# Kernel optimization log

Hardware: AMD Instinct MI355X
Metric: run time of the kernel (lower is better)

## Reference

```python
import jax, jax.numpy as jnp
import numpy as np

# Module config (matches init_kwargs)
SHAPE = (96, 128, 128)   # (D, H, W)
NUM_LAYERS = 2
K, S, P, DIL = 3, 2, 1, 1  # kernel, stride, padding, dilation (dilation=1)


def _sparse_maxpool(feat, mask):
    """One SparseMaxPool3d layer on a densified sparse tensor.

    feat: [B, D, H, W, C] float, inactive sites hold dtype-min
    mask: [B, D, H, W, 1] float 0/1 activity mask
    Max is taken only over ACTIVE input sites in each window (spconv semantics);
    an output site is active iff any input in its window is active.
    """
    neg = jnp.finfo(feat.dtype).min
    window = (1, K, K, K, 1)
    strides = (1, S, S, S, 1)
    pad = [(0, 0), (P, P), (P, P), (P, P), (0, 0)]
    masked = jnp.where(mask > 0, feat, neg)
    pooled = jax.lax.reduce_window(masked, neg, jax.lax.max, window, strides, pad)
    mask_out = jax.lax.reduce_window(mask, jnp.array(0, feat.dtype).item() * 0.0,
                                     jax.lax.max, window, strides, pad)
    return pooled, mask_out


def setup_inputs() -> dict:
    key = jax.random.key(0)
    k1, k2, k3, k4, k5 = jax.random.split(key, 5)
    N, C, B = 200000, 32, 2
    D, H, W = SHAPE
    features = jax.random.normal(k1, (N, C), dtype=jnp.float32)
    b = jax.random.randint(k2, (N,), 0, B)
    z = jax.random.randint(k3, (N,), 0, D)
    y = jax.random.randint(k4, (N,), 0, H)
    x = jax.random.randint(k5, (N,), 0, W)
    coors = jnp.stack([b, z, y, x], axis=1).astype(jnp.int32)
    return {"features": features, "coors": coors, "batch_size": B}


def reference(features, coors, batch_size):
    D, H, W = SHAPE
    C = features.shape[1]
    b, z, y, x = coors[:, 0], coors[:, 1], coors[:, 2], coors[:, 3]
    neg = jnp.finfo(features.dtype).min
    # Densify the sparse tensor (duplicate coords resolved by max, inactive = -inf)
    dense = jnp.full((batch_size, D, H, W, C), neg, features.dtype)
    dense = dense.at[b, z, y, x].max(features)
    mask = jnp.zeros((batch_size, D, H, W, 1), features.dtype).at[b, z, y, x].set(1.0)
    for _ in range(NUM_LAYERS):
        dense, mask = _sparse_maxpool(dense, mask)
    # Equivalent of SparseConvTensor.dense(): inactive output sites are 0
    return jnp.where(mask > 0, dense, jnp.zeros((), features.dtype))
```

## Files before the change

kernel.cpp:

```cpp
#include <hip/hip_runtime.h>
#include <cfloat>
#include <cstdint>

#define B_    2
#define OD    24
#define OH    32
#define OW    32
#define NC    32
#define NBINS (B_ * OD * OH * OW)
#define LINE  16
#define CAPR  15
#define OVF_CAP 100000
#define SCAN_T 1024
#define CHUNK  (NBINS / SCAN_T)

#define TZ 4
#define TY 4
#define TX 2
#define TCELLS (TZ*TY*TX)
#define NTZ (OD/TZ)
#define NTY (OH/TY)
#define NTX (OW/TX)
#define NTILES (B_*NTZ*NTY*NTX)
#define NBZ (TZ+1)
#define NBY (TY+1)
#define NBX (TX+1)
#define NB  (NBZ*NBY*NBX)
#define LIST_CAP 1280
#define DUMP (TCELLS*NC)


__global__ void k_zero(int* __restrict__ lines, int* __restrict__ ovf_n) {
    int i = blockIdx.x * blockDim.x + threadIdx.x;
    if (i < NBINS) lines[i * LINE] = 0;
    if (i == 0) *ovf_n = 0;
}

__global__ __launch_bounds__(256) void k_bin(const int* __restrict__ coors,
                                             int* __restrict__ lines,
                                             int* __restrict__ ovf_n,
                                             int2* __restrict__ ovf, int N) {
    int i = blockIdx.x * blockDim.x + threadIdx.x;
    if (i >= N) return;
    int4 cc = reinterpret_cast<const int4*>(coors)[i];
    int bin = (((cc.x * OD + (cc.y >> 2)) * OH + (cc.z >> 2)) * OW + (cc.w >> 2));
    int mask = 0xFF;
    if (!(cc.y & 3)) mask &= 0x55;
    if (!(cc.z & 3)) mask &= 0x33;
    if (!(cc.w & 3)) mask &= 0x0F;
    int rec = (i << 8) | mask;
    int pos = atomicAdd(&lines[bin * LINE], 1);
    if (pos < CAPR) {
        lines[bin * LINE + 1 + pos] = rec;
    } else {
        int o = atomicAdd(ovf_n, 1);
        if (o < OVF_CAP) ovf[o] = make_int2(bin, rec);
    }
}

__device__ __forceinline__ unsigned xform(float f) {
    unsigned u = __float_as_uint(f);
    return u ^ ((unsigned)((int)u >> 31) | 0x80000000u);
}
__device__ __forceinline__ float unxform(unsigned t) {
    return (t == 0u) ? 0.0f
           : __uint_as_float((t >> 31) ? (t ^ 0x80000000u) : ~t);
}

__global__ __launch_bounds__(512) void k_tile(const float* __restrict__ feat,
                                              const int* __restrict__ lines,
                                              const int* __restrict__ ovf_n,
                                              const int2* __restrict__ ovf,
                                              float4* __restrict__ out4) {
    __shared__ unsigned sm_out[TCELLS * NC + 32];
    __shared__ int2 list[LIST_CAP];
    __shared__ int sm_cursor;

    const int tid = threadIdx.x;
    int bid = blockIdx.x;
    int b  = (bid >= NTZ * NTY * NTX) ? 1 : 0;
    int r  = bid - b * (NTZ * NTY * NTX);
    int ti = r >> 7;
    int rr = r & 127;
    int tj = rr >> 4;
    int tl = rr & 15;
    const int tz0 = ti * TZ, ty0 = tj * TY, tx0 = tl * TX;

    if (tid == 0) sm_cursor = 0;
    for (int v = tid; v < TCELLS * NC + 32; v += 512) sm_out[v] = 0u;
    __syncthreads();

    if (tid < NB) {
        int rz  = tid / (NBY * NBX);
        int rem = tid - rz * (NBY * NBX);
        int ry  = rem / NBX;
        int rx  = rem - ry * NBX;
        int bz = tz0 - 1 + rz, by = ty0 - 1 + ry, bx = tx0 - 1 + rx;
        if ((bz | by | bx) >= 0) {
            int bin = ((b * OD + bz) * OH + by) * OW + bx;
            const int4* lp = (const int4*)(lines + bin * LINE);
            int4 q0 = lp[0], q1 = lp[1], q2 = lp[2], q3 = lp[3];
            int rbuf[16];
            *(int4*)&rbuf[0]  = q0; *(int4*)&rbuf[4]  = q1;
            *(int4*)&rbuf[8]  = q2; *(int4*)&rbuf[12] = q3;
            int cnt = rbuf[0]; if (cnt > CAPR) cnt = CAPR;
            int bi = rz - 1, bj = ry - 1, bl = rx - 1;
            int vm = 0xFF;
            if (bi < 0) vm &= 0xAA;  if (bi > TZ - 2) vm &= 0x55;
            if (bj < 0) vm &= 0xCC;  if (bj > TY - 2) vm &= 0x33;
            if (bl < 0) vm &= 0xF0;  if (bl > TX - 2) vm &= 0x0F;
            int cb = bi * (TY * TX) + bj * TX + bl;
#pragma unroll
            for (int rs = 0; rs < CAPR; ++rs) {
                if (rs < cnt) {
                    int rec = rbuf[rs + 1];
                    int fm = rec & vm & 0xFF;
                    if (fm) {
                        int pos = atomicAdd(&sm_cursor, 1);
                        if (pos < LIST_CAP)
                            list[pos] = make_int2((rec & ~0xFF) | fm, cb);
                    }
                }
            }
        }
    }
    int on = *ovf_n;
    if (on > 0 && tid == 0) {
        if (on > OVF_CAP) on = OVF_CAP;
        for (int e = 0; e < on; ++e) {
            int2 ov = ovf[e];
            int bx = ov.x & (OW - 1);
            int by = (ov.x >> 5) & (OH - 1);
            int rest = ov.x >> 10;
            int bb = (rest >= OD) ? 1 : 0;
            int bz = rest - bb * OD;
            if (bb != b) continue;
            int rz = bz - (tz0 - 1), ry = by - (ty0 - 1), rx = bx - (tx0 - 1);
            if (rz < 0 || rz >= NBZ || ry < 0 || ry >= NBY || rx < 0 || rx >= NBX) continue;
            int bi = rz - 1, bj = ry - 1, bl = rx - 1;
            int vm = 0xFF;
            if (bi < 0) vm &= 0xAA;  if (bi > TZ - 2) vm &= 0x55;
            if (bj < 0) vm &= 0xCC;  if (bj > TY - 2) vm &= 0x33;
            if (bl < 0) vm &= 0xF0;  if (bl > TX - 2) vm &= 0x0F;
            int fm = ov.y & vm & 0xFF;
            if (fm) {
                int pos = atomicAdd(&sm_cursor, 1);
                if (pos < LIST_CAP)
                    list[pos] = make_int2((ov.y & ~0xFF) | fm,
                                          bi * (TY * TX) + bj * TX + bl);
            }
        }
    }
    __syncthreads();
    int total = sm_cursor; if (total > LIST_CAP) total = LIST_CAP;

    const int s = tid >> 5;
    const int c = tid & 31;

    for (int j = s; j < total; j += 32) {
        int2 e0 = list[j];
        bool h1 = (j + 16) < total;
        int2 e1 = h1 ? list[j + 16] : make_int2(0, 0);
        float f0 = feat[(((unsigned)e0.x) >> 8) * NC + c];
        float f1 = feat[(((unsigned)e1.x) >> 8) * NC + c];
        unsigned t0 = xform(f0);
        unsigned t1 = xform(f1);
        int fm0 = e0.x & 0xFF, cb0 = e0.y;
        int fm1 = e1.x & 0xFF, cb1 = e1.y;
#pragma unroll
        for (int k = 0; k < 8; ++k) {
            const int koff = (k & 1) * (TY * TX) + ((k >> 1) & 1) * TX + ((k >> 2) & 1);
            int a0 = ((fm0 >> k) & 1) ? (cb0 + koff) * NC : DUMP;
            atomicMax(&sm_out[a0 + c], t0);
            int a1 = ((fm1 >> k) & 1) ? (cb1 + koff) * NC : DUMP;
            atomicMax(&sm_out[a1 + c], t1);
        }
    }
    __syncthreads();

    if (tid < TCELLS * NC / 4) {
        int cell = tid >> 3, quad = tid & 7;
        int i = cell >> 3, jj = (cell >> 1) & 3, l = cell & 1;
        uint4 uv = *(const uint4*)&sm_out[cell * NC + quad * 4];
        float4 o;
        o.x = unxform(uv.x); o.y = unxform(uv.y);
        o.z = unxform(uv.z); o.w = unxform(uv.w);
        out4[(((b * OD + tz0 + i) * OH + (ty0 + jj)) * OW + (tx0 + l)) * (NC / 4) + quad] = o;
    }
}


__global__ void k_hist(const int* __restrict__ coors, int* __restrict__ counts, int N) {
    int i = blockIdx.x * blockDim.x + threadIdx.x;
    if (i >= N) return;
    int4 cc = reinterpret_cast<const int4*>(coors)[i];
    int bin = (((cc.x * OD + (cc.y >> 2)) * OH + (cc.z >> 2)) * OW + (cc.w >> 2));
    atomicAdd(&counts[bin], 1);
}

__global__ void k_scan(const int* __restrict__ counts,
                       int2* __restrict__ binfo,
                       int* __restrict__ cursor) {
    __shared__ int lds[SCAN_T];
    int t = threadIdx.x;
    int base = t * CHUNK;
    int s = 0;
#pragma unroll
    for (int k = 0; k < CHUNK; ++k) s += counts[base + k];
    lds[t] = s;
    __syncthreads();
    for (int d = 1; d < SCAN_T; d <<= 1) {
        int v = (t >= d) ? lds[t - d] : 0;
        __syncthreads();
        lds[t] += v;
        __syncthreads();
    }
    int excl = (t == 0) ? 0 : lds[t - 1];
    for (int k = 0; k < CHUNK; ++k) {
        int i = base + k;
        int c = counts[i];
        binfo[i] = make_int2(excl, c);
        cursor[i] = excl;
        excl += c;
    }
}

__global__ void k_place(const int* __restrict__ coors, int* __restrict__ cursor,
                        int* __restrict__ records, int N) {
    int i = blockIdx.x * blockDim.x + threadIdx.x;
    if (i >= N) return;
    int4 cc = reinterpret_cast<const int4*>(coors)[i];
    int bin = (((cc.x * OD + (cc.y >> 2)) * OH + (cc.z >> 2)) * OW + (cc.w >> 2));
    int pos = atomicAdd(&cursor[bin], 1);
    records[pos] = (i << 6) | (cc.y & 3) | ((cc.z & 3) << 2) | ((cc.w & 3) << 4);
}

__global__ __launch_bounds__(256) void k_gather_fb(const float4* __restrict__ feat4,
                                                   const int2* __restrict__ binfo,
                                                   const int* __restrict__ records,
                                                   float4* __restrict__ out4, int N) {
    int tid  = blockIdx.x * blockDim.x + threadIdx.x;
    int wid  = tid >> 6;
    int lane = threadIdx.x & 63;
    int q    = lane >> 3;
    int cq   = lane & 7;

    int ox  = wid & (OW - 1);
    int oy  = (wid >> 5) & (OH - 1);
    int bzc = wid >> 10;
    int b   = (bzc >= OD) ? 1 : 0;
    int oz  = bzc - b * OD;

    int2 bi[8];
#pragma unroll
    for (int k = 0; k < 8; ++k) {
        const int lz = k & 1, ly = (k >> 1) & 1, lx = (k >> 2) & 1;
        int z2 = oz - lz, y2 = oy - ly, x2 = ox - lx;
        bool okbin = ((z2 | y2 | x2) >= 0);
        int bin = ((b * OD + z2) * OH + y2) * OW + x2;
        int2 v = binfo[okbin ? bin : 0];
        if (!okbin) { v.x = N; v.y = 0; }
        bi[k] = v;
    }

    int recs[8];
#pragma unroll
    for (int k = 0; k < 8; ++k) {
        int j = (q < bi[k].y) ? q : 0;
        recs[k] = records[bi[k].x + j];
    }

    float4 m = make_float4(-FLT_MAX, -FLT_MAX, -FLT_MAX, -FLT_MAX);
    int any = 0;
#pragma unroll
    for (int k = 0; k < 8; ++k) {
        int rec = recs[k];
        bool ok = (q < bi[k].y);
        if (k & 1) ok = ok && ((rec & 3)  != 0);
        if (k & 2) ok = ok && ((rec & 12) != 0);
        if (k & 4) ok = ok && ((rec & 48) != 0);
        if (ok) {
            float4 f = feat4[(rec >> 6) * (NC / 4) + cq];
            m.x = fmaxf(m.x, f.x); m.y = fmaxf(m.y, f.y);
            m.z = fmaxf(m.z, f.z); m.w = fmaxf(m.w, f.w);
            any = 1;
        }
    }

#pragma unroll
    for (int k = 0; k < 8; ++k) {
        for (int j0 = 8; j0 < bi[k].y; j0 += 8) {
            int j = j0 + q;
            bool ok = (j < bi[k].y);
            int rec = records[bi[k].x + (ok ? j : 0)];
            if (k & 1) ok = ok && ((rec & 3)  != 0);
            if (k & 2) ok = ok && ((rec & 12) != 0);
            if (k & 4) ok = ok && ((rec & 48) != 0);
            if (ok) {
                float4 f = feat4[(rec >> 6) * (NC / 4) + cq];
                m.x = fmaxf(m.x, f.x); m.y = fmaxf(m.y, f.y);
                m.z = fmaxf(m.z, f.z); m.w = fmaxf(m.w, f.w);
                any = 1;
            }
        }
    }

#pragma unroll
    for (int s = 8; s < 64; s <<= 1) {
        m.x = fmaxf(m.x, __shfl_xor(m.x, s, 64));
        m.y = fmaxf(m.y, __shfl_xor(m.y, s, 64));
        m.z = fmaxf(m.z, __shfl_xor(m.z, s, 64));
        m.w = fmaxf(m.w, __shfl_xor(m.w, s, 64));
    }
    bool active = (__ballot(any) != 0ULL);

    if (q == 0) {
        float4 z4 = make_float4(0.f, 0.f, 0.f, 0.f);
        out4[wid * (NC / 4) + cq] = active ? m : z4;
    }
}


extern "C" void kernel_launch(void* const* d_in, const int* in_sizes, int n_in,
                              void* d_out, int out_size, void* d_ws, size_t ws_size,
                              hipStream_t stream) {
    const float* feat  = (const float*)d_in[0];
    const int*   coors = (const int*)d_in[1];
    const int N = in_sizes[0] / NC;
    float* out = (float*)d_out;

    const size_t fast_ints = (size_t)NBINS * LINE + 8 + 2ull * OVF_CAP;
    if (ws_size >= fast_ints * sizeof(int)) {
        int*  lines = (int*)d_ws;
        int*  ovf_n = lines + NBINS * LINE;
        int2* ovf   = (int2*)(ovf_n + 8);

        k_zero<<<(NBINS + 255) / 256, 256, 0, stream>>>(lines, ovf_n);
        k_bin<<<(N + 255) / 256, 256, 0, stream>>>(coors, lines, ovf_n, ovf, N);
        k_tile<<<NTILES, 512, 0, stream>>>(feat, lines, ovf_n, (const int2*)ovf,
                                           (float4*)out);
    } else {
        int*  counts  = (int*)d_ws;
        int2* binfo   = (int2*)(counts + NBINS);
        int*  cursor  = (int*)(binfo + NBINS);
        int*  records = cursor + NBINS;

        hipMemsetAsync(counts, 0, NBINS * sizeof(int), stream);
        k_hist <<<(N + 255) / 256, 256, 0, stream>>>(coors, counts, N);
        k_scan <<<1, SCAN_T, 0, stream>>>(counts, binfo, cursor);
        k_place<<<(N + 255) / 256, 256, 0, stream>>>(coors, cursor, records, N);
        k_gather_fb<<<(NBINS * 64) / 256, 256, 0, stream>>>(
            (const float4*)feat, (const int2*)binfo, records, (float4*)out, N);
    }
}
```

Measured before the change: 46.52 us.

## Enlarge tile to 4x4x4 cells and batch list-slot reservation per bin

Doubles the output tile width in x so each block covers 64 cells. This cuts the halo overhead of re-reading neighboring bins and halves the block count. Each bin thread now reserves its list slots with one shared atomic instead of one per record, and entries past the list capacity are handled inline instead of dropped. The scatter loop processes four entries per iteration and skips masked atomics with branches instead of writing to a dump slot. The risks are more shared memory per block and lower occupancy, plus a slow inline fallback if the list overflows.

```diff
diff --git a/kernel.cpp b/kernel.cpp
--- a/kernel.cpp
+++ b/kernel.cpp
@@ -16,7 +16,7 @@
 
 #define TZ 4
 #define TY 4
-#define TX 2
+#define TX 4
 #define TCELLS (TZ*TY*TX)
 #define NTZ (OD/TZ)
 #define NTY (OH/TY)
@@ -26,8 +26,16 @@
 #define NBY (TY+1)
 #define NBX (TX+1)
 #define NB  (NBZ*NBY*NBX)
-#define LIST_CAP 1280
-#define DUMP (TCELLS*NC)
+#define LIST_CAP 1792
+
+__device__ __forceinline__ unsigned xform(float f) {
+    unsigned u = __float_as_uint(f);
+    return u ^ ((unsigned)((int)u >> 31) | 0x80000000u);
+}
+__device__ __forceinline__ float unxform(unsigned t) {
+    return (t == 0u) ? 0.0f
+           : __uint_as_float((t >> 31) ? (t ^ 0x80000000u) : ~t);
+}
 
 
 __global__ void k_zero(int* __restrict__ lines, int* __restrict__ ovf_n) {
@@ -58,36 +66,27 @@
     }
 }
 
-__device__ __forceinline__ unsigned xform(float f) {
-    unsigned u = __float_as_uint(f);
-    return u ^ ((unsigned)((int)u >> 31) | 0x80000000u);
-}
-__device__ __forceinline__ float unxform(unsigned t) {
-    return (t == 0u) ? 0.0f
-           : __uint_as_float((t >> 31) ? (t ^ 0x80000000u) : ~t);
-}
 
 __global__ __launch_bounds__(512) void k_tile(const float* __restrict__ feat,
                                               const int* __restrict__ lines,
                                               const int* __restrict__ ovf_n,
                                               const int2* __restrict__ ovf,
                                               float4* __restrict__ out4) {
-    __shared__ unsigned sm_out[TCELLS * NC + 32];
+    __shared__ unsigned sm_out[TCELLS * NC];
     __shared__ int2 list[LIST_CAP];
     __shared__ int sm_cursor;
 
+    const int t   = blockIdx.x;
     const int tid = threadIdx.x;
-    int bid = blockIdx.x;
-    int b  = (bid >= NTZ * NTY * NTX) ? 1 : 0;
-    int r  = bid - b * (NTZ * NTY * NTX);
-    int ti = r >> 7;
-    int rr = r & 127;
-    int tj = rr >> 4;
-    int tl = rr & 15;
-    const int tz0 = ti * TZ, ty0 = tj * TY, tx0 = tl * TX;
+    const int tx_ = t & (NTX - 1);
+    const int ty_ = (t >> 3) & (NTY - 1);
+    const int rest = t >> 6;
+    const int b   = (rest >= NTZ) ? 1 : 0;
+    const int tz_ = rest - b * NTZ;
+    const int tz0 = tz_ * TZ, ty0 = ty_ * TY, tx0 = tx_ * TX;
 
     if (tid == 0) sm_cursor = 0;
-    for (int v = tid; v < TCELLS * NC + 32; v += 512) sm_out[v] = 0u;
+    for (int v = tid; v < TCELLS * NC; v += 512) sm_out[v] = 0u;
     __syncthreads();
 
     if (tid < NB) {
@@ -110,20 +109,39 @@
             if (bj < 0) vm &= 0xCC;  if (bj > TY - 2) vm &= 0x33;
             if (bl < 0) vm &= 0xF0;  if (bl > TX - 2) vm &= 0x0F;
             int cb = bi * (TY * TX) + bj * TX + bl;
+            int nk = 0;
+#pragma unroll
+            for (int rs = 0; rs < CAPR; ++rs)
+                if (rs < cnt && (rbuf[rs + 1] & vm & 0xFF)) ++nk;
+            int pos = atomicAdd(&sm_cursor, nk);
 #pragma unroll
             for (int rs = 0; rs < CAPR; ++rs) {
                 if (rs < cnt) {
                     int rec = rbuf[rs + 1];
                     int fm = rec & vm & 0xFF;
                     if (fm) {
-                        int pos = atomicAdd(&sm_cursor, 1);
-                        if (pos < LIST_CAP)
+                        if (pos < LIST_CAP) {
                             list[pos] = make_int2((rec & ~0xFF) | fm, cb);
+                        } else {
+                            unsigned idx = ((unsigned)rec) >> 8;
+                            for (int c2 = 0; c2 < NC; ++c2) {
+                                unsigned tvv = xform(feat[idx * NC + c2]);
+#pragma unroll
+                                for (int k = 0; k < 8; ++k) {
+                                    const int koff = ((k & 1) * (TY * TX)
+                                        + ((k >> 1) & 1) * TX + ((k >> 2) & 1)) * NC;
+                                    if ((fm >> k) & 1)
+                                        atomicMax(&sm_out[(cb * NC) + koff + c2], tvv);
+                                }
+                            }
+                        }
+                        ++pos;
                     }
                 }
             }
         }
     }
+
     int on = *ovf_n;
     if (on > 0 && tid == 0) {
         if (on > OVF_CAP) on = OVF_CAP;
@@ -131,9 +149,9 @@
             int2 ov = ovf[e];
             int bx = ov.x & (OW - 1);
             int by = (ov.x >> 5) & (OH - 1);
-            int rest = ov.x >> 10;
-            int bb = (rest >= OD) ? 1 : 0;
-            int bz = rest - bb * OD;
+            int rest2 = ov.x >> 10;
+            int bb = (rest2 >= OD) ? 1 : 0;
+            int bz = rest2 - bb * OD;
             if (bb != b) continue;
             int rz = bz - (tz0 - 1), ry = by - (ty0 - 1), rx = bx - (tx0 - 1);
             if (rz < 0 || rz >= NBZ || ry < 0 || ry >= NBY || rx < 0 || rx >= NBX) continue;
@@ -157,35 +175,36 @@
     const int s = tid >> 5;
     const int c = tid & 31;
 
-    for (int j = s; j < total; j += 32) {
-        int2 e0 = list[j];
-        bool h1 = (j + 16) < total;
-        int2 e1 = h1 ? list[j + 16] : make_int2(0, 0);
-        float f0 = feat[(((unsigned)e0.x) >> 8) * NC + c];
-        float f1 = feat[(((unsigned)e1.x) >> 8) * NC + c];
-        unsigned t0 = xform(f0);
-        unsigned t1 = xform(f1);
-        int fm0 = e0.x & 0xFF, cb0 = e0.y;
-        int fm1 = e1.x & 0xFF, cb1 = e1.y;
+    for (int j0 = s; j0 < total; j0 += 64) {
+        int2 e0 = (j0      < total) ? list[j0]      : make_int2(0, 0);
+        int2 e1 = (j0 + 16 < total) ? list[j0 + 16] : make_int2(0, 0);
+        int2 e2 = (j0 + 32 < total) ? list[j0 + 32] : make_int2(0, 0);
+        int2 e3 = (j0 + 48 < total) ? list[j0 + 48] : make_int2(0, 0);
+        unsigned t0 = xform(feat[(((unsigned)e0.x) >> 8) * NC + c]);
+        unsigned t1 = xform(feat[(((unsigned)e1.x) >> 8) * NC + c]);
+        unsigned t2 = xform(feat[(((unsigned)e2.x) >> 8) * NC + c]);
+        unsigned t3 = xform(feat[(((unsigned)e3.x) >> 8) * NC + c]);
 #pragma unroll
         for (int k = 0; k < 8; ++k) {
-            const int koff = (k & 1) * (TY * TX) + ((k >> 1) & 1) * TX + ((k >> 2) & 1);
-            int a0 = ((fm0 >> k) & 1) ? (cb0 + koff) * NC : DUMP;
-            atomicMax(&sm_out[a0 + c], t0);
-            int a1 = ((fm1 >> k) & 1) ? (cb1 + koff) * NC : DUMP;
-            atomicMax(&sm_out[a1 + c], t1);
+            const int koff = ((k & 1) * (TY * TX) + ((k >> 1) & 1) * TX
+                           + ((k >> 2) & 1)) * NC + c;
+            if ((e0.x >> k) & 1) atomicMax(&sm_out[e0.y * NC + koff], t0);
+            if ((e1.x >> k) & 1) atomicMax(&sm_out[e1.y * NC + koff], t1);
+            if ((e2.x >> k) & 1) atomicMax(&sm_out[e2.y * NC + koff], t2);
+            if ((e3.x >> k) & 1) atomicMax(&sm_out[e3.y * NC + koff], t3);
         }
     }
     __syncthreads();
 
-    if (tid < TCELLS * NC / 4) {
-        int cell = tid >> 3, quad = tid & 7;
-        int i = cell >> 3, jj = (cell >> 1) & 3, l = cell & 1;
+    {
+        const int cell = tid >> 3, quad = tid & 7;
+        const int i = cell >> 4, jj = (cell >> 2) & 3, l = cell & 3;
         uint4 uv = *(const uint4*)&sm_out[cell * NC + quad * 4];
         float4 o;
         o.x = unxform(uv.x); o.y = unxform(uv.y);
         o.z = unxform(uv.z); o.w = unxform(uv.w);
-        out4[(((b * OD + tz0 + i) * OH + (ty0 + jj)) * OW + (tx0 + l)) * (NC / 4) + quad] = o;
+        out4[(((size_t)(b * OD + tz0 + i) * OH + (ty0 + jj)) * OW
+              + (tx0 + l)) * (NC / 4) + quad] = o;
     }
 }
 
```

Result: faster. 43.51 us (-6.5%).
